# Kernel optimization log

Hardware: AMD Instinct MI355X
Metric: run time of the kernel (lower is better)

## Reference

```python
import jax, jax.numpy as jnp
import numpy as np

B, L, D, H = 8, 1024, 768, 12
HD = D // H
EPS = 1e-5
R_EPS = 1e-12  # numerical guard for r at coincident positions


def setup_inputs() -> dict:
    key = jax.random.key(0)
    ks = jax.random.split(key, 8)
    x = jax.random.normal(ks[0], (B, L, D), dtype=jnp.float32)
    # 32x32 patch grid coordinates, same for every batch element
    g = jnp.arange(32, dtype=jnp.float32)
    yy, xx = jnp.meshgrid(g, g, indexing='ij')
    pos = jnp.broadcast_to(jnp.stack([yy.ravel(), xx.ravel()], axis=-1), (B, L, 2))
    w_norm = jnp.ones((D,), dtype=jnp.float32)
    w_in = 0.02 * jax.random.normal(ks[1], (3 * D, D), dtype=jnp.float32)
    b_in = jnp.zeros((3 * D,), dtype=jnp.float32)
    w_out = 0.02 * jax.random.normal(ks[2], (D, D), dtype=jnp.float32)
    b_out = jnp.zeros((D,), dtype=jnp.float32)
    # bias params [H, 6] = (o, c, w, p, delta, m) per init_bias_params
    o = jnp.zeros((H,), dtype=jnp.float32)
    c = 1.0 + 0.3 * jax.random.uniform(ks[3], (H,), dtype=jnp.float32)
    w = jnp.ones((H,), dtype=jnp.float32)
    p = jnp.zeros((H,), dtype=jnp.float32)
    delta = jax.random.normal(ks[4], (H,), dtype=jnp.float32)
    m = jnp.ones((H,), dtype=jnp.float32)
    bias_params = jnp.stack([o, c, w, p, delta, m], axis=-1)
    return {"x": x, "pos": pos, "w_norm": w_norm, "w_in": w_in, "b_in": b_in,
            "w_out": w_out, "b_out": b_out, "bias_params": bias_params}


def _bias_grid(pos, bias_params):
    # pos: [B, L, 2] -> bias: [B, H, L, L]
    o, c, w, p, delta, m = [bias_params[:, i].reshape(1, H, 1, 1) for i in range(6)]
    dist = pos[:, :, None, :] - pos[:, None, :, :]          # [B, Lq, Lk, 2]
    theta = jnp.arctan2(dist[..., 1], dist[..., 0])[:, None]  # [B, 1, Lq, Lk]
    r = jnp.sqrt(jnp.sum(dist * dist, axis=-1) + R_EPS)[:, None]
    term1 = jax.nn.relu(r - o) ** jnp.abs(c)
    term2 = 1.0 - jnp.abs(jnp.tanh(delta)) * (jnp.cos((theta - p) * w * 0.5) ** 2) ** jnp.abs(m)
    return term1 * term2


def reference(x, pos, w_norm, w_in, b_in, w_out, b_out, bias_params):
    bias = _bias_grid(pos, bias_params)                      # [B, H, L, L]
    # RMSNorm
    xn = x * jax.lax.rsqrt(jnp.mean(x * x, axis=-1, keepdims=True) + EPS) * w_norm
    qkv = xn @ w_in.T + b_in                                 # [B, L, 3D]
    q, k, v = jnp.split(qkv, 3, axis=-1)
    def heads(t):
        return t.reshape(B, L, H, HD).transpose(0, 2, 1, 3)  # [B, H, L, HD]
    q, k, v = heads(q), heads(k), heads(v)
    scores = jnp.einsum('bhqd,bhkd->bhqk', q, k) / jnp.sqrt(jnp.float32(HD)) + bias
    attn = jax.nn.softmax(scores, axis=-1)
    o = jnp.einsum('bhqk,bhkd->bhqd', attn, v)
    o = o.transpose(0, 2, 1, 3).reshape(B, L, D)
    return o @ w_out.T + b_out
```

## Files before the change

### kernel.cpp

```cpp
#include <hip/hip_runtime.h>

#define BB 8
#define LL 1024
#define DD 768
#define HH 12
#define HD 64

typedef short s16x8 __attribute__((ext_vector_type(8)));
typedef float f32x4 __attribute__((ext_vector_type(4)));
typedef unsigned int u32x4 __attribute__((ext_vector_type(4)));

static __device__ __forceinline__ unsigned short f2bf(float f){
  unsigned int u = __builtin_bit_cast(unsigned int, f);
  u = (u + 0x7FFFu + ((u >> 16) & 1u)) >> 16;
  return (unsigned short)u;
}

static __device__ __forceinline__ unsigned int cvtpk_bf(float a, float b){
  unsigned int r;
  asm("v_cvt_pk_bf16_f32 %0, %1, %2" : "=v"(r) : "v"(a), "v"(b));
  return r;
}

static __device__ __forceinline__ void swap32(unsigned int& a, unsigned int& b){
  asm("v_permlane32_swap_b32 %0, %1" : "+v"(a), "+v"(b));
}
static __device__ __forceinline__ void swap16(unsigned int& a, unsigned int& b){
  asm("v_permlane16_swap_b32 %0, %1" : "+v"(a), "+v"(b));
}

static __device__ __forceinline__ f32x4 mfma16(s16x8 a, s16x8 b, f32x4 c){
  return __builtin_amdgcn_mfma_f32_16x16x32_bf16(a, b, c, 0, 0, 0);
}

static __device__ __forceinline__ void gld_lds16(const void* g, void* l){
  __builtin_amdgcn_global_load_lds(
      (const __attribute__((address_space(1))) void*)g,
      (__attribute__((address_space(3))) void*)l, 16, 0, 0);
}

__global__ void cvt_kernel(const float* __restrict__ src, unsigned short* __restrict__ dst, int n4){
  int i = blockIdx.x*256 + threadIdx.x;
  if (i < n4){
    float4 v = ((const float4*)src)[i];
    ushort4 o;
    o.x = f2bf(v.x); o.y = f2bf(v.y); o.z = f2bf(v.z); o.w = f2bf(v.w);
    ((ushort4*)dst)[i] = o;
  }
}

__global__ void bias_table_kernel(const float* __restrict__ bp, float* __restrict__ table){
  int idx = blockIdx.x*256 + threadIdx.x;
  if (idx >= HH*3969) return;
  int hh = idx/3969, rem = idx - hh*3969;
  int dy = rem/63 - 31, dx = rem%63 - 31;
  float o  = bp[hh*6+0], c = bp[hh*6+1], w = bp[hh*6+2];
  float p  = bp[hh*6+3], dl = bp[hh*6+4], m = bp[hh*6+5];
  float theta = atan2f((float)dx, (float)dy);
  float r = sqrtf((float)(dy*dy + dx*dx) + 1e-12f);
  float t1 = powf(fmaxf(r - o, 0.0f), fabsf(c));
  float co = cosf((theta - p)*w*0.5f);
  float t2 = 1.0f - fabsf(tanhf(dl))*powf(co*co, fabsf(m));
  table[idx] = t1*t2*1.44269504f;
}

__global__ __launch_bounds__(64) void bmax_kernel(const float* __restrict__ table,
                                                  float* __restrict__ bmax){
  int qy = blockIdx.x, h = blockIdx.y;
  __shared__ float m1[63];
  int t = threadIdx.x;
  const float* tb = table + h*3969;
  if (t < 63){
    float m = -3.0e38f;
    #pragma unroll 4
    for (int row = qy; row < qy + 32; row++) m = fmaxf(m, tb[row*63 + t]);
    m1[t] = m;
  }
  __syncthreads();
  if (t < 32){
    float m = -3.0e38f;
    #pragma unroll 4
    for (int c = t; c < t + 32; c++) m = fmaxf(m, m1[c]);
    bmax[(h*32 + qy)*32 + t] = m;
  }
}

__global__ __launch_bounds__(256) void rmsnorm_kernel(const float* __restrict__ x,
                                                      const float* __restrict__ wn,
                                                      unsigned short* __restrict__ xn){
  int row = blockIdx.x, t = threadIdx.x;
  const float* xr = x + (size_t)row*DD;
  float v0 = xr[t], v1 = xr[t+256], v2 = xr[t+512];
  float ss = v0*v0 + v1*v1 + v2*v2;
  #pragma unroll
  for (int m = 1; m < 64; m <<= 1) ss += __shfl_xor(ss, m, 64);
  __shared__ float red[4];
  if ((t & 63) == 0) red[t >> 6] = ss;
  __syncthreads();
  float tot = red[0] + red[1] + red[2] + red[3];
  float sc = rsqrtf(tot*(1.0f/DD) + 1e-5f);
  unsigned short* xo = xn + (size_t)row*DD;
  xo[t]     = f2bf(v0*sc*wn[t]);
  xo[t+256] = f2bf(v1*sc*wn[t+256]);
  xo[t+512] = f2bf(v2*sc*wn[t+512]);
}

static __device__ __forceinline__ void storeC(float* p, float v){ *p = v; }
static __device__ __forceinline__ void storeC(unsigned short* p, float v){ *p = f2bf(v); }

template<int MODE, int TN, typename OutT>
__global__ __launch_bounds__(256) void gemm_bt_kernel(const unsigned short* __restrict__ A,
                                                      const unsigned short* __restrict__ B,
                                                      const float* __restrict__ bias,
                                                      OutT* __restrict__ C,
                                                      unsigned short* __restrict__ qp,
                                                      unsigned short* __restrict__ kp,
                                                      unsigned short* __restrict__ vp,
                                                      int M, int N, int K){
  constexpr int NT = TN/32;
  __shared__ __align__(16) unsigned short As[2][128*32];
  __shared__ __align__(16) unsigned short Bs[2][TN*32];
  int tid = threadIdx.x;
  int w = tid >> 6, lane = tid & 63, quad = lane >> 4, col = lane & 15;
  int wm = (w >> 1)*64, wn = (w & 1)*(TN/2);
  int bm = blockIdx.x*128, bn = blockIdx.y*TN;

  int srow = lane >> 2;
  int schunk = (lane & 3)*8;
  const unsigned short* ga0 = A + (size_t)(bm + w*32 + srow)*K + schunk;
  const unsigned short* ga1 = ga0 + (size_t)16*K;
  const unsigned short* gb0 = B + (size_t)(bn + w*(TN/4) + srow)*K + schunk;
  const unsigned short* gb1 = gb0 + (size_t)16*K;

  f32x4 acc[4][NT];
  #pragma unroll
  for (int mt = 0; mt < 4; mt++)
    #pragma unroll
    for (int nt = 0; nt < NT; nt++) acc[mt][nt] = (f32x4){0.f,0.f,0.f,0.f};

  gld_lds16(ga0, As[0] + (w*32)*32);
  gld_lds16(ga1, As[0] + (w*32 + 16)*32);
  gld_lds16(gb0, Bs[0] + (w*(TN/4))*32);
  if (TN == 128) gld_lds16(gb1, Bs[0] + (w*32 + 16)*32);

  int KT = K >> 5;
  for (int t = 0; t < KT; t++){
    int buf = t & 1;
    __syncthreads();
    if (t + 1 < KT){
      int kk = (t + 1)*32;
      gld_lds16(ga0 + kk, As[buf^1] + (w*32)*32);
      gld_lds16(ga1 + kk, As[buf^1] + (w*32 + 16)*32);
      gld_lds16(gb0 + kk, Bs[buf^1] + (w*(TN/4))*32);
      if (TN == 128) gld_lds16(gb1 + kk, Bs[buf^1] + (w*32 + 16)*32);
    }
    s16x8 af[4], bf[NT];
    #pragma unroll
    for (int mt = 0; mt < 4; mt++)
      af[mt] = *(const s16x8*)&As[buf][(wm + mt*16 + col)*32 + quad*8];
    #pragma unroll
    for (int nt = 0; nt < NT; nt++)
      bf[nt] = *(const s16x8*)&Bs[buf][(wn + nt*16 + col)*32 + quad*8];
    #pragma unroll
    for (int mt = 0; mt < 4; mt++)
      #pragma unroll
      for (int nt = 0; nt < NT; nt++)
        acc[mt][nt] = mfma16(af[mt], bf[nt], acc[mt][nt]);
  }

  #pragma unroll
  for (int mt = 0; mt < 4; mt++)
    #pragma unroll
    for (int nt = 0; nt < NT; nt++){
      int cl = bn + wn + nt*16 + col;
      float bv = bias[cl];
      #pragma unroll
      for (int r = 0; r < 4; r++){
        int rw = bm + wm + mt*16 + quad*4 + r;
        float v = acc[mt][nt][r] + bv;
        if (MODE == 0){
          storeC(&C[(size_t)rw*N + cl], v);
        } else {
          int part = cl >= 1536 ? 2 : (cl >= 768 ? 1 : 0);
          int hd = cl - part*768;
          int h = hd >> 6, d = hd & 63;
          int bb = rw >> 10, l = rw & 1023;
          size_t base = (((size_t)bb*HH + h)*LL + l)*64;
          unsigned short v16 = f2bf(v);
          if (part == 0)      qp[base + d] = v16;
          else if (part == 1) kp[base + ((((d>>3) ^ (l&7)) << 3) | (d & 7))] = v16;
          else                vp[base + d] = v16;
        }
      }
    }
}

__global__ __launch_bounds__(256) void vtrans_kernel(const unsigned short* __restrict__ vp,
                                                     unsigned short* __restrict__ vt2){
  int jt = blockIdx.x, bh = blockIdx.y;
  __shared__ unsigned short tile[32][68];
  int t = threadIdx.x;
  const unsigned short* src = vp + ((size_t)bh*LL + jt*32)*64;
  #pragma unroll
  for (int e = 0; e < 8; e++){
    int lin = t + 256*e;
    tile[lin >> 6][lin & 63] = src[lin];
  }
  __syncthreads();
  unsigned short* dst = vt2 + ((size_t)bh*32 + jt)*2048;
  #pragma unroll
  for (int e = 0; e < 8; e++){
    int lin = t + 256*e;
    dst[lin] = tile[lin & 31][lin >> 5];
  }
}

__global__ __launch_bounds__(256) void attn_kernel(const unsigned short* __restrict__ qp,
                                                   const unsigned short* __restrict__ kp,
                                                   const unsigned short* __restrict__ vt2,
                                                   const float* __restrict__ table,
                                                   const float* __restrict__ bmax,
                                                   const float* __restrict__ pos,
                                                   unsigned short* __restrict__ o_out){
  int i = blockIdx.x;
  int bh = (i >> 6)*8 + (i & 7);
  int qt = (i >> 3) & 7;
  int b = bh/HH, h = bh - b*HH;
  int tid = threadIdx.x, w = tid >> 6, lane = tid & 63, quad = lane >> 4, col = lane & 15;
  __shared__ float tl[3969];
  __shared__ int ky63[32];
  __shared__ __align__(16) unsigned short Ks[2][2048];
  __shared__ __align__(16) unsigned short Vs[2][2048];

  const unsigned short* kgp = kp  + (size_t)bh*65536;
  const unsigned short* vgp = vt2 + (size_t)bh*65536;
  int soff = w*512 + lane*8;

  gld_lds16(kgp + soff, &Ks[0][w*512]);
  gld_lds16(vgp + soff, &Vs[0][w*512]);

  for (int j = tid; j < 3969; j += 256) tl[j] = table[h*3969 + j];
  const float* pb = pos + (size_t)b*2048;
  if (tid < 32) ky63[tid] = 63*__float2int_rn(pb[tid*64]);
  __syncthreads();

  int qw = qt*128 + w*32;
  const unsigned short* qpb = qp + (size_t)bh*65536;
  s16x8 qa[2][2];
  int cq[2];
  f32x4 zb[2];
  #pragma unroll
  for (int g = 0; g < 2; g++){
    int q = qw + g*16 + col;
    size_t qo = (size_t)q*64 + quad*8;
    qa[g][0] = *(const s16x8*)(qpb + qo);
    qa[g][1] = *(const s16x8*)(qpb + qo + 32);
    int qy = __float2int_rn(pb[q*2]);
    int qx = __float2int_rn(pb[q*2 + 1]);
    cq[g] = qy*63 + qx + 1984 - quad*4;
    float neg = -5.5451774445f * bmax[(h*32 + qy)*32 + qx];
    zb[g] = (f32x4){neg, neg, neg, neg};
  }

  s16x8 ones;
  #pragma unroll
  for (int e = 0; e < 8; e++) ones[e] = (short)0x3F80;

  int sw = col & 7;
  int a_k0 = col*128 + ((quad    ) ^ sw)*16;
  int a_k1 = col*128 + ((quad + 4) ^ sw)*16;
  int a_k2 = a_k0 + 2048;
  int a_k3 = a_k1 + 2048;
  int a_v  = col*64 + quad*16;

  f32x4 o[2][4];
  f32x4 l_acc[2];
  #pragma unroll
  for (int g = 0; g < 2; g++){
    #pragma unroll
    for (int nt = 0; nt < 4; nt++) o[g][nt] = (f32x4){0.f,0.f,0.f,0.f};
    l_acc[g] = (f32x4){0.f,0.f,0.f,0.f};
  }

  for (int t = 0; t < 32; t++){
    int buf = t & 1;
    __syncthreads();
    if (t < 31){
      gld_lds16(kgp + (t+1)*2048 + soff, &Ks[buf^1][w*512]);
      gld_lds16(vgp + (t+1)*2048 + soff, &Vs[buf^1][w*512]);
    }
    const char* kb = (const char*)Ks[buf];
    const char* vb = (const char*)Vs[buf];
    s16x8 k0 = *(const s16x8*)(kb + a_k0);
    s16x8 k1 = *(const s16x8*)(kb + a_k1);
    s16x8 k2 = *(const s16x8*)(kb + a_k2);
    s16x8 k3 = *(const s16x8*)(kb + a_k3);
    s16x8 v0 = *(const s16x8*)(vb + a_v);
    s16x8 v1 = *(const s16x8*)(vb + a_v + 1024);
    s16x8 v2 = *(const s16x8*)(vb + a_v + 2048);
    s16x8 v3 = *(const s16x8*)(vb + a_v + 3072);
    int kyt = ky63[t];

    #pragma unroll
    for (int g = 0; g < 2; g++){
      f32x4 s_lo = mfma16(k0, qa[g][0], zb[g]);  s_lo = mfma16(k1, qa[g][1], s_lo);
      f32x4 s_hi = mfma16(k2, qa[g][0], zb[g]);  s_hi = mfma16(k3, qa[g][1], s_hi);
      int base = cq[g] - kyt;
      float pl[4], ph[4];
      #pragma unroll
      for (int r = 0; r < 4; r++){
        pl[r] = exp2f(__builtin_fmaf(s_lo[r], 0.18033688f, tl[base - r]));
        ph[r] = exp2f(__builtin_fmaf(s_hi[r], 0.18033688f, tl[base - r - 16]));
      }
      unsigned int wA = cvtpk_bf(pl[0], pl[1]);
      unsigned int wB = cvtpk_bf(pl[2], pl[3]);
      unsigned int wC = cvtpk_bf(ph[0], ph[1]);
      unsigned int wD = cvtpk_bf(ph[2], ph[3]);
      swap32(wA, wC);  swap32(wB, wD);
      swap16(wA, wC);  swap16(wB, wD);
      u32x4 pv4; pv4.x = wA; pv4.y = wB; pv4.z = wC; pv4.w = wD;
      s16x8 pf = __builtin_bit_cast(s16x8, pv4);
      l_acc[g] = mfma16(ones, pf, l_acc[g]);
      o[g][0] = mfma16(v0, pf, o[g][0]);
      o[g][1] = mfma16(v1, pf, o[g][1]);
      o[g][2] = mfma16(v2, pf, o[g][2]);
      o[g][3] = mfma16(v3, pf, o[g][3]);
    }
  }

  #pragma unroll
  for (int g = 0; g < 2; g++){
    float inv = 1.0f / l_acc[g][0];
    int q = qw + g*16 + col;
    unsigned short* orow = o_out + (size_t)(b*LL + q)*DD + h*64;
    #pragma unroll
    for (int nt = 0; nt < 4; nt++){
      uint2 pkd;
      pkd.x = cvtpk_bf(o[g][nt][0]*inv, o[g][nt][1]*inv);
      pkd.y = cvtpk_bf(o[g][nt][2]*inv, o[g][nt][3]*inv);
      *(uint2*)&orow[nt*16 + quad*4] = pkd;
    }
  }
}

extern "C" void kernel_launch(void* const* d_in, const int* in_sizes, int n_in,
                              void* d_out, int out_size, void* d_ws, size_t ws_size,
                              hipStream_t stream){
  const float* x      = (const float*)d_in[0];
  const float* pos    = (const float*)d_in[1];
  const float* w_norm = (const float*)d_in[2];
  const float* w_in   = (const float*)d_in[3];
  const float* b_in   = (const float*)d_in[4];
  const float* w_out  = (const float*)d_in[5];
  const float* b_out  = (const float*)d_in[6];
  const float* bp     = (const float*)d_in[7];

  char* ws = (char*)d_ws;
  unsigned short* xn    = (unsigned short*)(ws);
  unsigned short* winb  = (unsigned short*)(ws + 12582912);
  unsigned short* woutb = (unsigned short*)(ws + 16121856);
  unsigned short* qpb   = (unsigned short*)(ws + 17301504);
  unsigned short* kpb   = (unsigned short*)(ws + 29884416);
  unsigned short* vpb   = (unsigned short*)(ws + 42467328);
  unsigned short* vt2b  = (unsigned short*)(ws + 55050240);
  float*          table = (float*)        (ws + 67633152);
  unsigned short* ob    = (unsigned short*)(ws + 67823664);
  float*          bmaxp = (float*)        (ws);

  cvt_kernel<<<dim3((2304*768/4)/256), dim3(256), 0, stream>>>(w_in, winb, 2304*768/4);
  cvt_kernel<<<dim3((768*768/4)/256), dim3(256), 0, stream>>>(w_out, woutb, 768*768/4);
  bias_table_kernel<<<dim3((HH*3969 + 255)/256), dim3(256), 0, stream>>>(bp, table);
  rmsnorm_kernel<<<dim3(BB*LL), dim3(256), 0, stream>>>(x, w_norm, xn);
  gemm_bt_kernel<1, 128, unsigned short><<<dim3(64, 18), dim3(256), 0, stream>>>(
      xn, winb, b_in, (unsigned short*)nullptr, qpb, kpb, vpb, BB*LL, 3*DD, DD);
  bmax_kernel<<<dim3(32, HH), dim3(64), 0, stream>>>(table, bmaxp);
  vtrans_kernel<<<dim3(32, BB*HH), dim3(256), 0, stream>>>(vpb, vt2b);
  attn_kernel<<<dim3(768), dim3(256), 0, stream>>>(qpb, kpb, vt2b, table, bmaxp, pos, ob);
  gemm_bt_kernel<0, 64, float><<<dim3(64, 12), dim3(256), 0, stream>>>(
      ob, woutb, b_out, (float*)d_out, nullptr, nullptr, nullptr, BB*LL, DD, DD);
}
```

Measured before the change: 239.5 us.

## Triple-buffer LDS tiles with explicit vmcnt waits in GEMM and attention

Both the GEMM and attention kernels move from double to triple buffering of their LDS tiles. Loads are issued two iterations ahead, and __syncthreads is replaced by a partial s_waitcnt vmcnt plus a raw s_barrier, so one tile's loads can stay in flight during compute. The attention inner loop is also wrapped in s_setprio. The cost is more LDS per block, which may lower occupancy, and the correctness of the hand-counted vmcnt values depends on the exact number of outstanding loads.

```diff
diff --git a/kernel.cpp b/kernel.cpp
--- a/kernel.cpp
+++ b/kernel.cpp
@@ -118,8 +118,8 @@
                                                       unsigned short* __restrict__ vp,
                                                       int M, int N, int K){
   constexpr int NT = TN/32;
-  __shared__ __align__(16) unsigned short As[2][128*32];
-  __shared__ __align__(16) unsigned short Bs[2][TN*32];
+  __shared__ __align__(16) unsigned short As[3][128*32];
+  __shared__ __align__(16) unsigned short Bs[3][TN*32];
   int tid = threadIdx.x;
   int w = tid >> 6, lane = tid & 63, quad = lane >> 4, col = lane & 15;
   int wm = (w >> 1)*64, wn = (w & 1)*(TN/2);
@@ -132,40 +132,49 @@
   const unsigned short* gb0 = B + (size_t)(bn + w*(TN/4) + srow)*K + schunk;
   const unsigned short* gb1 = gb0 + (size_t)16*K;
 
+  auto stage = [&](int t, int b){
+    int kk = t*32;
+    gld_lds16(ga0 + kk, As[b] + (w*32)*32);
+    gld_lds16(ga1 + kk, As[b] + (w*32 + 16)*32);
+    gld_lds16(gb0 + kk, Bs[b] + (w*(TN/4))*32);
+    if (TN == 128) gld_lds16(gb1 + kk, Bs[b] + (w*32 + 16)*32);
+  };
+
   f32x4 acc[4][NT];
   #pragma unroll
   for (int mt = 0; mt < 4; mt++)
     #pragma unroll
     for (int nt = 0; nt < NT; nt++) acc[mt][nt] = (f32x4){0.f,0.f,0.f,0.f};
 
-  gld_lds16(ga0, As[0] + (w*32)*32);
-  gld_lds16(ga1, As[0] + (w*32 + 16)*32);
-  gld_lds16(gb0, Bs[0] + (w*(TN/4))*32);
-  if (TN == 128) gld_lds16(gb1, Bs[0] + (w*32 + 16)*32);
+  stage(0, 0);
+  stage(1, 1);
 
   int KT = K >> 5;
+  int buf = 0, nbuf = 2;
   for (int t = 0; t < KT; t++){
-    int buf = t & 1;
-    __syncthreads();
-    if (t + 1 < KT){
-      int kk = (t + 1)*32;
-      gld_lds16(ga0 + kk, As[buf^1] + (w*32)*32);
-      gld_lds16(ga1 + kk, As[buf^1] + (w*32 + 16)*32);
-      gld_lds16(gb0 + kk, Bs[buf^1] + (w*(TN/4))*32);
-      if (TN == 128) gld_lds16(gb1 + kk, Bs[buf^1] + (w*32 + 16)*32);
-    }
-    s16x8 af[4], bf[NT];
+    if (t < KT - 1){
+      if (TN == 128) asm volatile("s_waitcnt vmcnt(4)" ::: "memory");
+      else           asm volatile("s_waitcnt vmcnt(3)" ::: "memory");
+    } else {
+      asm volatile("s_waitcnt vmcnt(0)" ::: "memory");
+    }
+    __builtin_amdgcn_s_barrier();
+    asm volatile("" ::: "memory");
+    if (t + 2 < KT) stage(t + 2, nbuf);
+    s16x8 af[4], bfr[NT];
     #pragma unroll
     for (int mt = 0; mt < 4; mt++)
       af[mt] = *(const s16x8*)&As[buf][(wm + mt*16 + col)*32 + quad*8];
     #pragma unroll
     for (int nt = 0; nt < NT; nt++)
-      bf[nt] = *(const s16x8*)&Bs[buf][(wn + nt*16 + col)*32 + quad*8];
+      bfr[nt] = *(const s16x8*)&Bs[buf][(wn + nt*16 + col)*32 + quad*8];
     #pragma unroll
     for (int mt = 0; mt < 4; mt++)
       #pragma unroll
       for (int nt = 0; nt < NT; nt++)
-        acc[mt][nt] = mfma16(af[mt], bf[nt], acc[mt][nt]);
+        acc[mt][nt] = mfma16(af[mt], bfr[nt], acc[mt][nt]);
+    buf  = (buf  == 2) ? 0 : buf  + 1;
+    nbuf = (nbuf == 2) ? 0 : nbuf + 1;
   }
 
   #pragma unroll
@@ -229,15 +238,17 @@
   int tid = threadIdx.x, w = tid >> 6, lane = tid & 63, quad = lane >> 4, col = lane & 15;
   __shared__ float tl[3969];
   __shared__ int ky63[32];
-  __shared__ __align__(16) unsigned short Ks[2][2048];
-  __shared__ __align__(16) unsigned short Vs[2][2048];
+  __shared__ __align__(16) unsigned short Ks[3][2048];
+  __shared__ __align__(16) unsigned short Vs[3][2048];
 
   const unsigned short* kgp = kp  + (size_t)bh*65536;
   const unsigned short* vgp = vt2 + (size_t)bh*65536;
   int soff = w*512 + lane*8;
 
-  gld_lds16(kgp + soff, &Ks[0][w*512]);
-  gld_lds16(vgp + soff, &Vs[0][w*512]);
+  gld_lds16(kgp + soff,        &Ks[0][w*512]);
+  gld_lds16(vgp + soff,        &Vs[0][w*512]);
+  gld_lds16(kgp + 2048 + soff, &Ks[1][w*512]);
+  gld_lds16(vgp + 2048 + soff, &Vs[1][w*512]);
 
   for (int j = tid; j < 3969; j += 256) tl[j] = table[h*3969 + j];
   const float* pb = pos + (size_t)b*2048;
@@ -282,12 +293,15 @@
     l_acc[g] = (f32x4){0.f,0.f,0.f,0.f};
   }
 
+  int buf = 0, nbuf = 2;
   for (int t = 0; t < 32; t++){
-    int buf = t & 1;
-    __syncthreads();
-    if (t < 31){
-      gld_lds16(kgp + (t+1)*2048 + soff, &Ks[buf^1][w*512]);
-      gld_lds16(vgp + (t+1)*2048 + soff, &Vs[buf^1][w*512]);
+    if (t < 31) asm volatile("s_waitcnt vmcnt(2)" ::: "memory");
+    else        asm volatile("s_waitcnt vmcnt(0)" ::: "memory");
+    __builtin_amdgcn_s_barrier();
+    asm volatile("" ::: "memory");
+    if (t + 2 < 32){
+      gld_lds16(kgp + (t+2)*2048 + soff, &Ks[nbuf][w*512]);
+      gld_lds16(vgp + (t+2)*2048 + soff, &Vs[nbuf][w*512]);
     }
     const char* kb = (const char*)Ks[buf];
     const char* vb = (const char*)Vs[buf];
@@ -301,6 +315,7 @@
     s16x8 v3 = *(const s16x8*)(vb + a_v + 3072);
     int kyt = ky63[t];
 
+    __builtin_amdgcn_s_setprio(1);
     #pragma unroll
     for (int g = 0; g < 2; g++){
       f32x4 s_lo = mfma16(k0, qa[g][0], zb[g]);  s_lo = mfma16(k1, qa[g][1], s_lo);
@@ -326,6 +341,9 @@
       o[g][2] = mfma16(v2, pf, o[g][2]);
       o[g][3] = mfma16(v3, pf, o[g][3]);
     }
+    __builtin_amdgcn_s_setprio(0);
+    buf  = (buf  == 2) ? 0 : buf  + 1;
+    nbuf = (nbuf == 2) ? 0 : nbuf + 1;
   }
 
   #pragma unroll
```

Result: no change. 244.1 us (+1.9%).
